# Optimization experiments

Hardware: AMD Instinct MI355X
Metric: run time of the kernel (lower is better)

## Reference

```python
import jax, jax.numpy as jnp
import numpy as np

B, E, C, Fdim, T = 8, 36, 4, 32, 2048
EDGE_DIM, NODE_DIM, NUM_NODES, NUM_CLASSES = 64, 128, 12, 9
# edges: all (i, j) with i in 0..5, j in 6..11, in loop order
U = np.repeat(np.arange(6), 6)
V = np.tile(np.arange(6, 12), 6)


def _p(key, shape, scale=0.05):
    return jax.random.normal(key, shape, jnp.float32) * scale


def setup_inputs():
    ks = iter(jax.random.split(jax.random.key(0), 64))
    nxt = lambda: next(ks)
    inp = {}
    inp["x"] = jax.random.normal(nxt(), (B, E, C, Fdim, T), jnp.float32)
    inp["conv1_w"] = _p(nxt(), (16, C, 3, 3)); inp["conv1_b"] = _p(nxt(), (16,))
    inp["bn1_s"] = jnp.ones((16,)); inp["bn1_b"] = jnp.zeros((16,))
    inp["bn1_m"] = jnp.zeros((16,)); inp["bn1_v"] = jnp.ones((16,))
    inp["se1_w1"] = _p(nxt(), (4, 16)); inp["se1_b1"] = _p(nxt(), (4,))
    inp["se1_w2"] = _p(nxt(), (16, 4)); inp["se1_b2"] = _p(nxt(), (16,))
    inp["conv2_w"] = _p(nxt(), (32, 16, 3, 3)); inp["conv2_b"] = _p(nxt(), (32,))
    inp["bn2_s"] = jnp.ones((32,)); inp["bn2_b"] = jnp.zeros((32,))
    inp["bn2_m"] = jnp.zeros((32,)); inp["bn2_v"] = jnp.ones((32,))
    inp["se2_w1"] = _p(nxt(), (8, 32)); inp["se2_b1"] = _p(nxt(), (8,))
    inp["se2_w2"] = _p(nxt(), (32, 8)); inp["se2_b2"] = _p(nxt(), (32,))
    inp["conv3_w"] = _p(nxt(), (64, 32, 3, 3)); inp["conv3_b"] = _p(nxt(), (64,))
    inp["bn3_s"] = jnp.ones((64,)); inp["bn3_b"] = jnp.zeros((64,))
    inp["bn3_m"] = jnp.zeros((64,)); inp["bn3_v"] = jnp.ones((64,))
    inp["edge_fc_w"] = _p(nxt(), (EDGE_DIM, 64)); inp["edge_fc_b"] = _p(nxt(), (EDGE_DIM,))
    inp["edge_w"] = _p(nxt(), (E,), 1.0)  # learnable_edge_weights
    inp["e2n_w"] = _p(nxt(), (NODE_DIM, EDGE_DIM)); inp["e2n_b"] = _p(nxt(), (NODE_DIM,))
    inp["attn1_w"] = _p(nxt(), (NODE_DIM // 2, NODE_DIM)); inp["attn1_b"] = _p(nxt(), (NODE_DIM // 2,))
    inp["attn2_w"] = _p(nxt(), (1, NODE_DIM // 2))
    inp["cls_w"] = _p(nxt(), (NUM_CLASSES, NODE_DIM)); inp["cls_b"] = _p(nxt(), (NUM_CLASSES,))
    inp["reg_w"] = _p(nxt(), (3, NODE_DIM)); inp["reg_b"] = _p(nxt(), (3,))
    return inp


def _conv(x, w, b, stride):
    y = jax.lax.conv_general_dilated(x, w, window_strides=stride,
        padding=[(1, 1), (1, 1)], dimension_numbers=("NCHW", "OIHW", "NCHW"))
    return y + b[None, :, None, None]


def _bn(x, s, b, m, v):
    # eval-mode BatchNorm2d (running stats)
    inv = s * jax.lax.rsqrt(v + 1e-5)
    return (x - m[None, :, None, None]) * inv[None, :, None, None] + b[None, :, None, None]


def _maxpool2(x):
    return jax.lax.reduce_window(x, -jnp.inf, jax.lax.max,
        (1, 1, 2, 2), (1, 1, 2, 2), "VALID")


def _se(x, w1, b1, w2, b2):
    y = x.mean(axis=(2, 3))                      # [N, C]
    y = jax.nn.relu(y @ w1.T + b1)
    y = jax.nn.sigmoid(y @ w2.T + b2)
    return x * y[:, :, None, None]


def _forward(x, conv1_w, conv1_b, bn1_s, bn1_b, bn1_m, bn1_v,
             se1_w1, se1_b1, se1_w2, se1_b2,
             conv2_w, conv2_b, bn2_s, bn2_b, bn2_m, bn2_v,
             se2_w1, se2_b1, se2_w2, se2_b2,
             conv3_w, conv3_b, bn3_s, bn3_b, bn3_m, bn3_v,
             edge_fc_w, edge_fc_b, edge_w, e2n_w, e2n_b,
             attn1_w, attn1_b, attn2_w, cls_w, cls_b, reg_w, reg_b):
    h = x.reshape(B * E, C, Fdim, T)
    h = jax.nn.relu(_bn(_conv(h, conv1_w, conv1_b, (1, 2)), bn1_s, bn1_b, bn1_m, bn1_v))
    h = _se(_maxpool2(h), se1_w1, se1_b1, se1_w2, se1_b2)
    h = jax.nn.relu(_bn(_conv(h, conv2_w, conv2_b, (1, 2)), bn2_s, bn2_b, bn2_m, bn2_v))
    h = _se(_maxpool2(h), se2_w1, se2_b1, se2_w2, se2_b2)
    h = jax.nn.relu(_bn(_conv(h, conv3_w, conv3_b, (1, 2)), bn3_s, bn3_b, bn3_m, bn3_v))
    h = h.mean(axis=(2, 3))                      # AdaptiveAvgPool2d(1) -> [B*E, 64]
    edge_feat = jax.nn.relu(h @ edge_fc_w.T + edge_fc_b).reshape(B, E, EDGE_DIM)

    # spatial GNN: weighted edge feats scatter-added to both endpoints
    w = jax.nn.softplus(edge_w)[None, :, None]   # [1, E, 1]
    wef = edge_feat * w                          # [B, E, D]
    node = jnp.zeros((B, NUM_NODES, EDGE_DIM), edge_feat.dtype)
    node = node.at[:, U].add(wef).at[:, V].add(wef)
    node = jax.nn.relu(node @ e2n_w.T + e2n_b)   # [B, 12, NODE_DIM]

    # attention pooling
    scores = jnp.tanh(node @ attn1_w.T + attn1_b) @ attn2_w.T   # [B, 12, 1]
    aw = jax.nn.softmax(scores, axis=1)
    ea = aw[:, U, 0] * aw[:, V, 0]               # [B, E]
    ea = ea / (ea.sum(axis=1, keepdims=True) + 1e-8)
    g = (node * aw).sum(axis=1)                  # [B, NODE_DIM]
    return (g @ reg_w.T + reg_b, g @ cls_w.T + cls_b, ea)


def reference(x, conv1_w, conv1_b, bn1_s, bn1_b, bn1_m, bn1_v,
              se1_w1, se1_b1, se1_w2, se1_b2,
              conv2_w, conv2_b, bn2_s, bn2_b, bn2_m, bn2_v,
              se2_w1, se2_b1, se2_w2, se2_b2,
              conv3_w, conv3_b, bn3_s, bn3_b, bn3_m, bn3_v,
              edge_fc_w, edge_fc_b, edge_w, e2n_w, e2n_b,
              attn1_w, attn1_b, attn2_w, cls_w, cls_b, reg_w, reg_b):
    return _forward(x, conv1_w, conv1_b, bn1_s, bn1_b, bn1_m, bn1_v,
                    se1_w1, se1_b1, se1_w2, se1_b2,
                    conv2_w, conv2_b, bn2_s, bn2_b, bn2_m, bn2_v,
                    se2_w1, se2_b1, se2_w2, se2_b2,
                    conv3_w, conv3_b, bn3_s, bn3_b, bn3_m, bn3_v,
                    edge_fc_w, edge_fc_b, edge_w, e2n_w, e2n_b,
                    attn1_w, attn1_b, attn2_w, cls_w, cls_b, reg_w, reg_b)
```

## Files before the change

### kernel.cpp

```cpp
#include <hip/hip_runtime.h>
#include <math.h>


#define GLOAD_LDS(src, dst) \
  __builtin_amdgcn_global_load_lds( \
      (const __attribute__((address_space(1))) void*)(src), \
      (__attribute__((address_space(3))) void*)(dst), 16, 0, 0)

__global__ void k_fold1(const float* __restrict__ w, const float* __restrict__ bs,
                        const float* __restrict__ bv, float* __restrict__ wf1)
{
  int i = blockIdx.x * blockDim.x + threadIdx.x;
  if (i < 576) {
    int co = i / 36, r = i % 36;
    float s = bs[co] * rsqrtf(bv[co] + 1e-5f);
    wf1[r * 16 + co] = w[i] * s;
  }
}

__global__ void k_fold2(const float* __restrict__ w, const float* __restrict__ bs,
                        const float* __restrict__ bv, const float* __restrict__ s1,
                        float* __restrict__ wf2)
{
  int n = blockIdx.x;
  const float* s1n = s1 + n * 16;
  for (int i = threadIdx.x; i < 4608; i += 256) {
    int co = i / 144, r = i % 144, ci = r / 9;
    float s = bs[co] * rsqrtf(bv[co] + 1e-5f);
    wf2[(size_t)n * 4608 + r * 32 + co] = w[i] * s * s1n[ci];
  }
}

__global__ __launch_bounds__(256) void k_conv1(
    const float* __restrict__ x, const float* __restrict__ wf1,
    const float* __restrict__ cb, const float* __restrict__ bs,
    const float* __restrict__ bb, const float* __restrict__ bm,
    const float* __restrict__ bv,
    float* __restrict__ h1, float* __restrict__ sesum)
{
  int bid = blockIdx.x;
  int colq = bid & 3, chunk = (bid >> 2) & 1, n = bid >> 3;
  __shared__ float tile[4][6][520];
  __shared__ float bi[16];

  const float* xn = x + (size_t)n * 4 * 32 * 2048;
  const int cbase = colq * 512;
  int tid = threadIdx.x;
  if (tid < 16) {
    int c = tid;
    float s = bs[c] * rsqrtf(bv[c] + 1e-5f);
    bi[c] = bb[c] + (cb[c] - bm[c]) * s;
  }
  int wv = tid >> 6, l = tid & 63;
  const int P0 = chunk * 8;
  {
#pragma unroll
    for (int j = 0; j < 8; j++) {
      int idx = wv * 8 + j;
      int ci = idx >> 3, rowidx = (idx >> 1) & 3, half = idx & 1;
      int ih = 2 * P0 - 1 + rowidx;
      int slot = ((ih % 6) + 6) % 6;
      int ihc = min(max(ih, 0), 31);
      const float* src =
          xn + ((size_t)ci * 32 + ihc) * 2048 + cbase + half * 256 + 4 * l;
      GLOAD_LDS(src, &tile[ci][slot][4 + half * 256 + 4 * l]);
    }
    if (tid < 16) {
      int ri = tid & 3, ci = tid >> 2;
      int ih2 = 2 * P0 - 1 + ri, slot2 = ((ih2 % 6) + 6) % 6;
      int ihc2 = min(max(ih2, 0), 31);
      tile[ci][slot2][3] =
          colq ? xn[((size_t)ci * 32 + ihc2) * 2048 + cbase - 1] : 0.f;
    }
  }
  __syncthreads();

  int cog = tid >> 7, tl = tid & 127;
  const int cobu = __builtin_amdgcn_readfirstlane(cog * 8);
  float sloc[8] = {0.f, 0.f, 0.f, 0.f, 0.f, 0.f, 0.f, 0.f};

#pragma unroll 1
  for (int pl = 0; pl < 8; pl++) {
    int p = P0 + pl;
    if (pl < 7) {
#pragma unroll
      for (int j = 0; j < 4; j++) {
        int idx = wv * 4 + j;
        int ci = idx >> 2, rsel = (idx >> 1) & 1, half = idx & 1;
        int ih = 2 * p + 3 + rsel;
        int slot = ih % 6;
        int ihc = min(ih, 31);
        const float* src =
            xn + ((size_t)ci * 32 + ihc) * 2048 + cbase + half * 256 + 4 * l;
        GLOAD_LDS(src, &tile[ci][slot][4 + half * 256 + 4 * l]);
      }
      if (tid < 8) {
        int rs2 = tid & 1, ci2 = tid >> 1;
        int ih2 = 2 * p + 3 + rs2, slot2 = ih2 % 6, ihc2 = min(ih2, 31);
        tile[ci2][slot2][3] =
            colq ? xn[((size_t)ci2 * 32 + ihc2) * 2048 + cbase - 1] : 0.f;
      }
    }
    float acc[2][2][8];
#pragma unroll
    for (int cr = 0; cr < 2; cr++)
#pragma unroll
      for (int cc = 0; cc < 2; cc++)
#pragma unroll
        for (int k = 0; k < 8; k++) acc[cr][cc][k] = 0.f;
    const bool ok0 = (p > 0), ok3 = (p < 15);
    int slots[4];
#pragma unroll
    for (int r = 0; r < 4; r++) {
      int ih = 2 * p - 1 + r;
      slots[r] = ((ih % 6) + 6) % 6;
    }
#pragma unroll 1
    for (int ci = 0; ci < 4; ci++) {
      float strip[4][5];
#pragma unroll
      for (int r = 0; r < 4; r++) {
        bool ok = (r == 0) ? ok0 : ((r == 3) ? ok3 : true);
        if (ok) {
          float4 vA = *reinterpret_cast<const float4*>(&tile[ci][slots[r]][4 * tl]);
          float4 vB = *reinterpret_cast<const float4*>(&tile[ci][slots[r]][4 * tl + 4]);
          strip[r][0] = vA.w;
          strip[r][1] = vB.x; strip[r][2] = vB.y; strip[r][3] = vB.z; strip[r][4] = vB.w;
        } else {
          strip[r][0] = strip[r][1] = strip[r][2] = strip[r][3] = strip[r][4] = 0.f;
        }
      }
      const float* wci = wf1 + ci * 9 * 16 + cobu;
#pragma unroll
      for (int kh = 0; kh < 3; kh++) {
#pragma unroll
        for (int kw = 0; kw < 3; kw++) {
          const float4* wq = reinterpret_cast<const float4*>(wci + (kh * 3 + kw) * 16);
          float4 w0 = wq[0], w1 = wq[1];
          float wr[8] = {w0.x, w0.y, w0.z, w0.w, w1.x, w1.y, w1.z, w1.w};
#pragma unroll
          for (int cr = 0; cr < 2; cr++) {
            float v0 = strip[cr + kh][kw], v1 = strip[cr + kh][2 + kw];
#pragma unroll
            for (int k = 0; k < 8; k++) {
              acc[cr][0][k] = fmaf(v0, wr[k], acc[cr][0][k]);
              acc[cr][1][k] = fmaf(v1, wr[k], acc[cr][1][k]);
            }
          }
        }
      }
    }
    int pc = colq * 128 + tl;
#pragma unroll
    for (int k = 0; k < 8; k++) {
      float m = fmaxf(fmaxf(acc[0][0][k], acc[0][1][k]),
                      fmaxf(acc[1][0][k], acc[1][1][k]));
      float po = fmaxf(m + bi[cobu + k], 0.f);
      h1[(((size_t)n * 16 + cobu + k) * 16 + p) * 512 + pc] = po;
      sloc[k] += po;
    }
    __syncthreads();
  }
#pragma unroll
  for (int k = 0; k < 8; k++) {
    float v = sloc[k];
    for (int off = 32; off; off >>= 1) v += __shfl_down(v, off);
    if (l == 0) atomicAdd(&sesum[n * 16 + cobu + k], v);
  }
}

__global__ void k_se(const float* __restrict__ sesum, int C, int Cr, float invcnt,
                     const float* __restrict__ w1, const float* __restrict__ b1,
                     const float* __restrict__ w2, const float* __restrict__ b2,
                     float* __restrict__ s)
{
  int n = blockIdx.x * blockDim.x + threadIdx.x;
  if (n >= 288) return;
  float y[32], t[8];
  for (int c = 0; c < C; c++) y[c] = sesum[n * C + c] * invcnt;
  for (int r = 0; r < Cr; r++) {
    float a = b1[r];
    for (int c = 0; c < C; c++) a += y[c] * w1[r * C + c];
    t[r] = fmaxf(a, 0.f);
  }
  for (int c = 0; c < C; c++) {
    float a = b2[c];
    for (int r = 0; r < Cr; r++) a += t[r] * w2[c * Cr + r];
    s[n * C + c] = 1.f / (1.f + expf(-a));
  }
}

__global__ __launch_bounds__(256) void k_conv2(
    const float* __restrict__ h1, const float* __restrict__ wf2,
    const float* __restrict__ cb, const float* __restrict__ bs,
    const float* __restrict__ bb, const float* __restrict__ bm,
    const float* __restrict__ bv,
    float* __restrict__ h2, float* __restrict__ sesum)
{
  int bid = blockIdx.x;
  int ph = bid & 7, n = bid >> 3;
  __shared__ float tile[2][2][4][520];
  __shared__ float bi[32];

  if (threadIdx.x < 32) {
    int c = threadIdx.x;
    float s = bs[c] * rsqrtf(bv[c] + 1e-5f);
    bi[c] = bb[c] + (cb[c] - bm[c]) * s;
  }
  if (threadIdx.x >= 64 && threadIdx.x < 128) {
    int t2 = threadIdx.x - 64;
    int b = t2 >> 5, ci = (t2 >> 4) & 1, r = (t2 >> 2) & 3, k = t2 & 3;
    tile[b][ci][r][k] = 0.f;
  }

  const float* hn = h1 + (size_t)n * 16 * 16 * 512;
  const float* wfn = wf2 + (size_t)n * 4608;
  int wv = threadIdx.x >> 6, l = threadIdx.x & 63;

  auto stage = [&](int c, int b) {
#pragma unroll
    for (int j = 0; j < 4; j++) {
      int idx = 4 * wv + j;
      int ci_l = idx >> 3, r = (idx >> 1) & 3, half = idx & 1;
      int ci = 2 * c + ci_l;
      int ih = min(max(2 * ph - 1 + r, 0), 15);
      const float* src = hn + ((size_t)ci * 16 + ih) * 512 + half * 256 + 4 * l;
      GLOAD_LDS(src, &tile[b][ci_l][r][4 + half * 256 + 4 * l]);
    }
  };

  stage(0, 0);
  __syncthreads();

  int cog = threadIdx.x >> 7, tl = threadIdx.x & 127;
  const int cobu = __builtin_amdgcn_readfirstlane(cog * 16);
  const bool ok0 = (ph > 0), ok3 = (ph < 7);
  float acc[2][2][16];
#pragma unroll
  for (int cr = 0; cr < 2; cr++)
#pragma unroll
    for (int cc = 0; cc < 2; cc++)
#pragma unroll
      for (int k = 0; k < 16; k++) acc[cr][cc][k] = 0.f;

#pragma unroll 1
  for (int c = 0; c < 8; c++) {
    if (c < 7) stage(c + 1, (c + 1) & 1);
    const int b = c & 1;
#pragma unroll 1
    for (int ci_l = 0; ci_l < 2; ci_l++) {
      int cg = 2 * c + ci_l;
      float strip[4][5];
#pragma unroll
      for (int r = 0; r < 4; r++) {
        bool ok = (r == 0) ? ok0 : ((r == 3) ? ok3 : true);
        if (ok) {
          float4 vA = *reinterpret_cast<const float4*>(&tile[b][ci_l][r][4 * tl]);
          float4 vB = *reinterpret_cast<const float4*>(&tile[b][ci_l][r][4 * tl + 4]);
          strip[r][0] = vA.w;
          strip[r][1] = vB.x; strip[r][2] = vB.y; strip[r][3] = vB.z; strip[r][4] = vB.w;
        } else {
          strip[r][0] = strip[r][1] = strip[r][2] = strip[r][3] = strip[r][4] = 0.f;
        }
      }
      const float* wci = wfn + cg * 9 * 32 + cobu;
#pragma unroll
      for (int kh = 0; kh < 3; kh++) {
#pragma unroll
        for (int kw = 0; kw < 3; kw++) {
          const float4* wq = reinterpret_cast<const float4*>(wci + (kh * 3 + kw) * 32);
          float4 w0 = wq[0], w1 = wq[1], w2 = wq[2], w3 = wq[3];
          float wr[16] = {w0.x, w0.y, w0.z, w0.w, w1.x, w1.y, w1.z, w1.w,
                          w2.x, w2.y, w2.z, w2.w, w3.x, w3.y, w3.z, w3.w};
#pragma unroll
          for (int cr = 0; cr < 2; cr++) {
            float v0 = strip[cr + kh][kw], v1 = strip[cr + kh][2 + kw];
#pragma unroll
            for (int k = 0; k < 16; k++) {
              acc[cr][0][k] = fmaf(v0, wr[k], acc[cr][0][k]);
              acc[cr][1][k] = fmaf(v1, wr[k], acc[cr][1][k]);
            }
          }
        }
      }
    }
    if (c < 7) __syncthreads();
  }

#pragma unroll
  for (int k = 0; k < 16; k++) {
    float m = fmaxf(fmaxf(acc[0][0][k], acc[0][1][k]),
                    fmaxf(acc[1][0][k], acc[1][1][k]));
    float po = fmaxf(m + bi[cobu + k], 0.f);
    h2[(((size_t)n * 32 + cobu + k) * 8 + ph) * 128 + tl] = po;
    float v = po;
    for (int off = 32; off; off >>= 1) v += __shfl_down(v, off);
    if (l == 0) atomicAdd(&sesum[n * 32 + cobu + k], v);
  }
}

__global__ __launch_bounds__(256) void k_conv3(
    const float* __restrict__ h2, const float* __restrict__ w,
    const float* __restrict__ cb, const float* __restrict__ bs,
    const float* __restrict__ bb, const float* __restrict__ bm,
    const float* __restrict__ bv,
    const float* __restrict__ s2, float* __restrict__ h3)
{
  int bid = blockIdx.x;
  int n = bid >> 2, cog = bid & 3;
  int hh = threadIdx.x >> 5, t = threadIdx.x & 31;
  __shared__ float tile[8][8][128];
  __shared__ float wl[32][3][3][16];
  __shared__ float bi[16];
  __shared__ float red[4][16];
  const float* s2n = s2 + n * 32;
  for (int i = threadIdx.x; i < 4608; i += 256) {
    int k = i / 288, r = i % 288, ci = r / 9, kk = r % 9;
    int co = cog * 16 + k;
    float s = bs[co] * rsqrtf(bv[co] + 1e-5f);
    wl[ci][kk / 3][kk % 3][k] = w[(size_t)co * 288 + r] * s * s2n[ci];
  }
  if (threadIdx.x < 16) {
    int c = cog * 16 + threadIdx.x;
    float s = bs[c] * rsqrtf(bv[c] + 1e-5f);
    bi[threadIdx.x] = bb[c] + (cb[c] - bm[c]) * s;
  }
  const float* hn = h2 + (size_t)n * 32 * 8 * 128;
  int wv = threadIdx.x >> 6, l = threadIdx.x & 63;
  const int aoff = t ? 4 * t - 4 : 0;
  float acc[2][16];
#pragma unroll
  for (int cc = 0; cc < 2; cc++)
#pragma unroll
    for (int k = 0; k < 16; k++) acc[cc][k] = 0.f;

#pragma unroll 1
  for (int c = 0; c < 4; c++) {
    for (int i = 0; i < 8; i++) {
      int pair = wv * 8 + i;
      int ci_l = pair >> 2, r2 = (pair & 3) * 2;
      int ci = c * 8 + ci_l;
      const float* src = hn + ((size_t)ci * 8 + r2) * 128 + 4 * l;
      GLOAD_LDS(src, &tile[ci_l][r2][4 * l]);
    }
    __syncthreads();
#pragma unroll 1
    for (int ci_l = 0; ci_l < 8; ci_l++) {
      int cg = c * 8 + ci_l;
      float strip[3][5];
#pragma unroll
      for (int r = 0; r < 3; r++) {
        int ih = hh - 1 + r;
        if (ih >= 0 && ih <= 7) {
          float4 vB = *reinterpret_cast<const float4*>(&tile[ci_l][ih][4 * t]);
          float4 vA = *reinterpret_cast<const float4*>(&tile[ci_l][ih][aoff]);
          strip[r][0] = t ? vA.w : 0.f;
          strip[r][1] = vB.x; strip[r][2] = vB.y; strip[r][3] = vB.z; strip[r][4] = vB.w;
        } else {
          strip[r][0] = strip[r][1] = strip[r][2] = strip[r][3] = strip[r][4] = 0.f;
        }
      }
#pragma unroll
      for (int kh = 0; kh < 3; kh++) {
#pragma unroll
        for (int kw = 0; kw < 3; kw++) {
          const float4* wp = reinterpret_cast<const float4*>(&wl[cg][kh][kw][0]);
          float4 w0 = wp[0], w1 = wp[1], w2 = wp[2], w3 = wp[3];
          float wr[16] = {w0.x, w0.y, w0.z, w0.w, w1.x, w1.y, w1.z, w1.w,
                          w2.x, w2.y, w2.z, w2.w, w3.x, w3.y, w3.z, w3.w};
          float v0 = strip[kh][kw], v1 = strip[kh][2 + kw];
#pragma unroll
          for (int k = 0; k < 16; k++) {
            acc[0][k] = fmaf(v0, wr[k], acc[0][k]);
            acc[1][k] = fmaf(v1, wr[k], acc[1][k]);
          }
        }
      }
    }
    __syncthreads();
  }
#pragma unroll
  for (int k = 0; k < 16; k++)
    acc[0][k] = fmaxf(acc[0][k] + bi[k], 0.f) + fmaxf(acc[1][k] + bi[k], 0.f);
#pragma unroll
  for (int k = 0; k < 16; k++) {
    float v = acc[0][k];
    for (int off = 32; off; off >>= 1) v += __shfl_down(v, off);
    if (l == 0) red[wv][k] = v;
  }
  __syncthreads();
  if (threadIdx.x < 16) {
    int k = threadIdx.x;
    float tt = red[0][k] + red[1][k] + red[2][k] + red[3][k];
    h3[n * 64 + cog * 16 + k] = tt * (1.f / 512.f);
  }
}

__global__ __launch_bounds__(256) void k_head(
    const float* __restrict__ h3,
    const float* __restrict__ efw, const float* __restrict__ efb,
    const float* __restrict__ ew,
    const float* __restrict__ e2nw, const float* __restrict__ e2nb,
    const float* __restrict__ a1w, const float* __restrict__ a1b,
    const float* __restrict__ a2w,
    const float* __restrict__ clsw, const float* __restrict__ clsb,
    const float* __restrict__ regw, const float* __restrict__ regb,
    float* __restrict__ out)
{
  int b = blockIdx.x;
  int tid = threadIdx.x;
  __shared__ float ef[36][64];
  __shared__ float nin[12][64];
  __shared__ float nd[12][128];
  __shared__ float tmp[12][64];
  __shared__ float spw[36], aw[12], scv[12], g[128], ea[36];
  if (tid < 36) {
    float xw = ew[tid];
    spw[tid] = (xw > 20.f) ? xw : log1pf(expf(xw));
  }
  __syncthreads();
  for (int idx = tid; idx < 36 * 64; idx += 256) {
    int e = idx >> 6, d = idx & 63;
    const float* hr = h3 + (size_t)(b * 36 + e) * 64;
    const float* wr = efw + d * 64;
    float a = efb[d];
    for (int k = 0; k < 64; k++) a += hr[k] * wr[k];
    ef[e][d] = fmaxf(a, 0.f) * spw[e];
  }
  __syncthreads();
  for (int idx = tid; idx < 12 * 64; idx += 256) {
    int j = idx >> 6, d = idx & 63;
    float a = 0.f;
    if (j < 6) { for (int i = 0; i < 6; i++) a += ef[j * 6 + i][d]; }
    else       { for (int i = 0; i < 6; i++) a += ef[i * 6 + (j - 6)][d]; }
    nin[j][d] = a;
  }
  __syncthreads();
  for (int idx = tid; idx < 12 * 128; idx += 256) {
    int j = idx >> 7, d = idx & 127;
    const float* wr = e2nw + d * 64;
    float a = e2nb[d];
    for (int k = 0; k < 64; k++) a += nin[j][k] * wr[k];
    nd[j][d] = fmaxf(a, 0.f);
  }
  __syncthreads();
  for (int idx = tid; idx < 12 * 64; idx += 256) {
    int j = idx >> 6, hh = idx & 63;
    const float* wr = a1w + hh * 128;
    float a = a1b[hh];
    for (int k = 0; k < 128; k++) a += nd[j][k] * wr[k];
    tmp[j][hh] = tanhf(a) * a2w[hh];
  }
  __syncthreads();
  if (tid < 12) {
    float a = 0.f;
    for (int h = 0; h < 64; h++) a += tmp[tid][h];
    scv[tid] = a;
  }
  __syncthreads();
  if (tid == 0) {
    float m = scv[0];
    for (int j = 1; j < 12; j++) m = fmaxf(m, scv[j]);
    float s = 0.f;
    for (int j = 0; j < 12; j++) { float z = expf(scv[j] - m); aw[j] = z; s += z; }
    float inv = 1.f / s;
    for (int j = 0; j < 12; j++) aw[j] *= inv;
    float rs = 0.f;
    for (int e = 0; e < 36; e++) { float r = aw[e / 6] * aw[6 + e % 6]; ea[e] = r; rs += r; }
    float inv2 = 1.f / (rs + 1e-8f);
    for (int e = 0; e < 36; e++) ea[e] *= inv2;
  }
  __syncthreads();
  if (tid < 36) out[96 + b * 36 + tid] = ea[tid];
  if (tid < 128) {
    float a = 0.f;
    for (int j = 0; j < 12; j++) a += nd[j][tid] * aw[j];
    g[tid] = a;
  }
  __syncthreads();
  if (tid < 3) {
    const float* wr = regw + tid * 128;
    float a = regb[tid];
    for (int k = 0; k < 128; k++) a += g[k] * wr[k];
    out[b * 3 + tid] = a;
  }
  if (tid >= 64 && tid < 73) {
    int i = tid - 64;
    const float* wr = clsw + i * 128;
    float a = clsb[i];
    for (int k = 0; k < 128; k++) a += g[k] * wr[k];
    out[24 + b * 9 + i] = a;
  }
}

extern "C" void kernel_launch(void* const* d_in, const int* in_sizes, int n_in,
                              void* d_out, int out_size, void* d_ws, size_t ws_size,
                              hipStream_t stream) {
  const float* x      = (const float*)d_in[0];
  const float* c1w    = (const float*)d_in[1];
  const float* c1b    = (const float*)d_in[2];
  const float* bn1s   = (const float*)d_in[3];
  const float* bn1b   = (const float*)d_in[4];
  const float* bn1m   = (const float*)d_in[5];
  const float* bn1v   = (const float*)d_in[6];
  const float* se1w1  = (const float*)d_in[7];
  const float* se1b1  = (const float*)d_in[8];
  const float* se1w2  = (const float*)d_in[9];
  const float* se1b2  = (const float*)d_in[10];
  const float* c2w    = (const float*)d_in[11];
  const float* c2b    = (const float*)d_in[12];
  const float* bn2s   = (const float*)d_in[13];
  const float* bn2b   = (const float*)d_in[14];
  const float* bn2m   = (const float*)d_in[15];
  const float* bn2v   = (const float*)d_in[16];
  const float* se2w1  = (const float*)d_in[17];
  const float* se2b1  = (const float*)d_in[18];
  const float* se2w2  = (const float*)d_in[19];
  const float* se2b2  = (const float*)d_in[20];
  const float* c3w    = (const float*)d_in[21];
  const float* c3b    = (const float*)d_in[22];
  const float* bn3s   = (const float*)d_in[23];
  const float* bn3b   = (const float*)d_in[24];
  const float* bn3m   = (const float*)d_in[25];
  const float* bn3v   = (const float*)d_in[26];
  const float* efw    = (const float*)d_in[27];
  const float* efb    = (const float*)d_in[28];
  const float* ew     = (const float*)d_in[29];
  const float* e2nw   = (const float*)d_in[30];
  const float* e2nb   = (const float*)d_in[31];
  const float* a1w    = (const float*)d_in[32];
  const float* a1b    = (const float*)d_in[33];
  const float* a2w    = (const float*)d_in[34];
  const float* clsw   = (const float*)d_in[35];
  const float* clsb   = (const float*)d_in[36];
  const float* regw   = (const float*)d_in[37];
  const float* regb   = (const float*)d_in[38];

  float* ws = (float*)d_ws;
  float* h1     = ws;
  float* h2     = h1 + 37748736;
  float* sesum1 = h2 + 9437184;
  float* s1     = sesum1 + 4608;
  float* sesum2 = s1 + 4608;
  float* s2     = sesum2 + 9216;
  float* h3     = s2 + 9216;
  float* wf1    = h3 + 18432;
  float* wf2    = wf1 + 576;

  hipMemsetAsync(sesum1, 0, 4608 * sizeof(float), stream);
  hipMemsetAsync(sesum2, 0, 9216 * sizeof(float), stream);

  k_fold1<<<3, 192, 0, stream>>>(c1w, bn1s, bn1v, wf1);
  k_conv1<<<288 * 8, 256, 0, stream>>>(x, wf1, c1b, bn1s, bn1b, bn1m, bn1v, h1, sesum1);
  k_se<<<5, 64, 0, stream>>>(sesum1, 16, 4, 1.f / 8192.f, se1w1, se1b1, se1w2, se1b2, s1);
  k_fold2<<<288, 256, 0, stream>>>(c2w, bn2s, bn2v, s1, wf2);
  k_conv2<<<288 * 8, 256, 0, stream>>>(h1, wf2, c2b, bn2s, bn2b, bn2m, bn2v, h2, sesum2);
  k_se<<<5, 64, 0, stream>>>(sesum2, 32, 8, 1.f / 1024.f, se2w1, se2b1, se2w2, se2b2, s2);
  k_conv3<<<288 * 4, 256, 0, stream>>>(h2, c3w, c3b, bn3s, bn3b, bn3m, bn3v, s2, h3);
  k_head<<<8, 256, 0, stream>>>(h3, efw, efb, ew, e2nw, e2nb, a1w, a1b, a2w,
                                clsw, clsb, regw, regb, (float*)d_out);
}
```

Measured before the change: 474.7 us.

## Prefold conv3 weights in separate kernel, widen conv3 to 32 channels, fuse memsets

```diff
diff --git a/kernel.cpp b/kernel.cpp
--- a/kernel.cpp
+++ b/kernel.cpp
@@ -8,7 +8,8 @@
       (__attribute__((address_space(3))) void*)(dst), 16, 0, 0)
 
 __global__ void k_fold1(const float* __restrict__ w, const float* __restrict__ bs,
-                        const float* __restrict__ bv, float* __restrict__ wf1)
+                        const float* __restrict__ bv, float* __restrict__ wf1,
+                        float* __restrict__ sesum1)
 {
   int i = blockIdx.x * blockDim.x + threadIdx.x;
   if (i < 576) {
@@ -16,11 +17,12 @@
     float s = bs[co] * rsqrtf(bv[co] + 1e-5f);
     wf1[r * 16 + co] = w[i] * s;
   }
+  if (i < 4608) sesum1[i] = 0.f;
 }
 
 __global__ void k_fold2(const float* __restrict__ w, const float* __restrict__ bs,
                         const float* __restrict__ bv, const float* __restrict__ s1,
-                        float* __restrict__ wf2)
+                        float* __restrict__ wf2, float* __restrict__ sesum2)
 {
   int n = blockIdx.x;
   const float* s1n = s1 + n * 16;
@@ -28,6 +30,21 @@
     int co = i / 144, r = i % 144, ci = r / 9;
     float s = bs[co] * rsqrtf(bv[co] + 1e-5f);
     wf2[(size_t)n * 4608 + r * 32 + co] = w[i] * s * s1n[ci];
+  }
+  if (threadIdx.x < 32) sesum2[n * 32 + threadIdx.x] = 0.f;
+}
+
+__global__ void k_fold3(const float* __restrict__ w, const float* __restrict__ bs,
+                        const float* __restrict__ bv, const float* __restrict__ s2,
+                        float* __restrict__ wf3)
+{
+  int n = blockIdx.x;
+  const float* s2n = s2 + n * 32;
+  for (int i = threadIdx.x; i < 18432; i += 256) {
+    int co = i / 288, r = i % 288, ci = r / 9;
+    float s = bs[co] * rsqrtf(bv[co] + 1e-5f);
+    wf3[(size_t)n * 18432 + r * 64 + co] =
+        w[(size_t)co * 288 + r] * s * s2n[ci];
   }
 }
 
@@ -300,39 +317,32 @@
 }
 
 __global__ __launch_bounds__(256) void k_conv3(
-    const float* __restrict__ h2, const float* __restrict__ w,
+    const float* __restrict__ h2, const float* __restrict__ wf3,
     const float* __restrict__ cb, const float* __restrict__ bs,
     const float* __restrict__ bb, const float* __restrict__ bm,
-    const float* __restrict__ bv,
-    const float* __restrict__ s2, float* __restrict__ h3)
+    const float* __restrict__ bv, float* __restrict__ h3)
 {
   int bid = blockIdx.x;
-  int n = bid >> 2, cog = bid & 3;
+  int n = bid >> 1, cog = bid & 1;
   int hh = threadIdx.x >> 5, t = threadIdx.x & 31;
   __shared__ float tile[8][8][128];
-  __shared__ float wl[32][3][3][16];
-  __shared__ float bi[16];
-  __shared__ float red[4][16];
-  const float* s2n = s2 + n * 32;
-  for (int i = threadIdx.x; i < 4608; i += 256) {
-    int k = i / 288, r = i % 288, ci = r / 9, kk = r % 9;
-    int co = cog * 16 + k;
-    float s = bs[co] * rsqrtf(bv[co] + 1e-5f);
-    wl[ci][kk / 3][kk % 3][k] = w[(size_t)co * 288 + r] * s * s2n[ci];
-  }
-  if (threadIdx.x < 16) {
-    int c = cog * 16 + threadIdx.x;
+  __shared__ float bi[32];
+  __shared__ float red[4][32];
+  if (threadIdx.x < 32) {
+    int c = cog * 32 + threadIdx.x;
     float s = bs[c] * rsqrtf(bv[c] + 1e-5f);
     bi[threadIdx.x] = bb[c] + (cb[c] - bm[c]) * s;
   }
   const float* hn = h2 + (size_t)n * 32 * 8 * 128;
+  const float* wfn = wf3 + (size_t)n * 18432;
+  const int cobu = __builtin_amdgcn_readfirstlane(cog * 32);
   int wv = threadIdx.x >> 6, l = threadIdx.x & 63;
   const int aoff = t ? 4 * t - 4 : 0;
-  float acc[2][16];
+  float acc[2][32];
 #pragma unroll
   for (int cc = 0; cc < 2; cc++)
 #pragma unroll
-    for (int k = 0; k < 16; k++) acc[cc][k] = 0.f;
+    for (int k = 0; k < 32; k++) acc[cc][k] = 0.f;
 
 #pragma unroll 1
   for (int c = 0; c < 4; c++) {
@@ -360,17 +370,21 @@
           strip[r][0] = strip[r][1] = strip[r][2] = strip[r][3] = strip[r][4] = 0.f;
         }
       }
+      const float* wci = wfn + cg * 9 * 64 + cobu;
 #pragma unroll
       for (int kh = 0; kh < 3; kh++) {
 #pragma unroll
         for (int kw = 0; kw < 3; kw++) {
-          const float4* wp = reinterpret_cast<const float4*>(&wl[cg][kh][kw][0]);
-          float4 w0 = wp[0], w1 = wp[1], w2 = wp[2], w3 = wp[3];
-          float wr[16] = {w0.x, w0.y, w0.z, w0.w, w1.x, w1.y, w1.z, w1.w,
-                          w2.x, w2.y, w2.z, w2.w, w3.x, w3.y, w3.z, w3.w};
+          const float4* wq = reinterpret_cast<const float4*>(wci + (kh * 3 + kw) * 64);
+          float4 w0 = wq[0], w1 = wq[1], w2 = wq[2], w3 = wq[3];
+          float4 w4 = wq[4], w5 = wq[5], w6 = wq[6], w7 = wq[7];
+          float wr[32] = {w0.x, w0.y, w0.z, w0.w, w1.x, w1.y, w1.z, w1.w,
+                          w2.x, w2.y, w2.z, w2.w, w3.x, w3.y, w3.z, w3.w,
+                          w4.x, w4.y, w4.z, w4.w, w5.x, w5.y, w5.z, w5.w,
+                          w6.x, w6.y, w6.z, w6.w, w7.x, w7.y, w7.z, w7.w};
           float v0 = strip[kh][kw], v1 = strip[kh][2 + kw];
 #pragma unroll
-          for (int k = 0; k < 16; k++) {
+          for (int k = 0; k < 32; k++) {
             acc[0][k] = fmaf(v0, wr[k], acc[0][k]);
             acc[1][k] = fmaf(v1, wr[k], acc[1][k]);
           }
@@ -380,19 +394,19 @@
     __syncthreads();
   }
 #pragma unroll
-  for (int k = 0; k < 16; k++)
+  for (int k = 0; k < 32; k++)
     acc[0][k] = fmaxf(acc[0][k] + bi[k], 0.f) + fmaxf(acc[1][k] + bi[k], 0.f);
 #pragma unroll
-  for (int k = 0; k < 16; k++) {
+  for (int k = 0; k < 32; k++) {
     float v = acc[0][k];
     for (int off = 32; off; off >>= 1) v += __shfl_down(v, off);
     if (l == 0) red[wv][k] = v;
   }
   __syncthreads();
-  if (threadIdx.x < 16) {
+  if (threadIdx.x < 32) {
     int k = threadIdx.x;
     float tt = red[0][k] + red[1][k] + red[2][k] + red[3][k];
-    h3[n * 64 + cog * 16 + k] = tt * (1.f / 512.f);
+    h3[n * 64 + cobu + k] = tt * (1.f / 512.f);
   }
 }
 
@@ -546,17 +560,16 @@
   float* h3     = s2 + 9216;
   float* wf1    = h3 + 18432;
   float* wf2    = wf1 + 576;
-
-  hipMemsetAsync(sesum1, 0, 4608 * sizeof(float), stream);
-  hipMemsetAsync(sesum2, 0, 9216 * sizeof(float), stream);
-
-  k_fold1<<<3, 192, 0, stream>>>(c1w, bn1s, bn1v, wf1);
+  float* wf3    = wf2 + 1327104;
+
+  k_fold1<<<18, 256, 0, stream>>>(c1w, bn1s, bn1v, wf1, sesum1);
   k_conv1<<<288 * 8, 256, 0, stream>>>(x, wf1, c1b, bn1s, bn1b, bn1m, bn1v, h1, sesum1);
   k_se<<<5, 64, 0, stream>>>(sesum1, 16, 4, 1.f / 8192.f, se1w1, se1b1, se1w2, se1b2, s1);
-  k_fold2<<<288, 256, 0, stream>>>(c2w, bn2s, bn2v, s1, wf2);
+  k_fold2<<<288, 256, 0, stream>>>(c2w, bn2s, bn2v, s1, wf2, sesum2);
   k_conv2<<<288 * 8, 256, 0, stream>>>(h1, wf2, c2b, bn2s, bn2b, bn2m, bn2v, h2, sesum2);
   k_se<<<5, 64, 0, stream>>>(sesum2, 32, 8, 1.f / 1024.f, se2w1, se2b1, se2w2, se2b2, s2);
-  k_conv3<<<288 * 4, 256, 0, stream>>>(h2, c3w, c3b, bn3s, bn3b, bn3m, bn3v, s2, h3);
+  k_fold3<<<288, 256, 0, stream>>>(c3w, bn3s, bn3v, s2, wf3);
+  k_conv3<<<288 * 2, 256, 0, stream>>>(h2, wf3, c3b, bn3s, bn3b, bn3m, bn3v, h3);
   k_head<<<8, 256, 0, stream>>>(h3, efw, efb, ew, e2nw, e2nb, a1w, a1b, a2w,
                                 clsw, clsb, regw, regb, (float*)d_out);
 }
```

Result: slower. 500.8 us (+5.5%).
